# Kernel tuning notes

Hardware: AMD Instinct MI355X
Metric: run time of the kernel (lower is better)

Reference implementation:

```python
import jax, jax.numpy as jnp
import numpy as np

N, E, G, H = 4096, 8192, 64, 128  # nodes, edges, graphs, hidden dim
NODE_DIM, EDGE_DIM = 11, 5


def _linear_params(key, fan_in, fan_out):
    kw, kb = jax.random.split(key)
    s = 1.0 / np.sqrt(fan_in)
    w = jax.random.uniform(kw, (fan_in, fan_out), minval=-s, maxval=s, dtype=jnp.float32)
    b = jax.random.uniform(kb, (fan_out,), minval=-s, maxval=s, dtype=jnp.float32)
    return w, b


def setup_inputs() -> dict:
    key = jax.random.key(0)
    ks = jax.random.split(key, 10)
    x = jax.random.normal(ks[0], (N, NODE_DIM), dtype=jnp.float32)
    edge_attr = jax.random.normal(ks[1], (E, EDGE_DIM), dtype=jnp.float32)
    edge_index = jax.random.randint(ks[2], (2, E), 0, N, dtype=jnp.int64)
    batch = jnp.sort(jax.random.randint(ks[3], (N,), 0, G, dtype=jnp.int64))
    # preprocess MLP: node_dim -> 128 -> 128
    p1_w, p1_b = _linear_params(ks[4], NODE_DIM, H)
    p2_w, p2_b = _linear_params(ks[5], H, H)
    # edge net: edge_dim -> 128 -> 256 -> 128 -> 128*128 (ReLU between, none after last)
    e1_w, e1_b = _linear_params(ks[6], EDGE_DIM, 128)
    e2_w, e2_b = _linear_params(ks[7], 128, 256)
    e3_w, e3_b = _linear_params(ks[8], 256, 128)
    e4_w, e4_b = _linear_params(ks[9], 128, H * H)
    return {"x": x, "edge_attr": edge_attr, "edge_index": edge_index, "batch": batch,
            "p1_w": p1_w, "p1_b": p1_b, "p2_w": p2_w, "p2_b": p2_b,
            "e1_w": e1_w, "e1_b": e1_b, "e2_w": e2_w, "e2_b": e2_b,
            "e3_w": e3_w, "e3_b": e3_b, "e4_w": e4_w, "e4_b": e4_b}


def reference(x, edge_attr, edge_index, batch,
              p1_w, p1_b, p2_w, p2_b,
              e1_w, e1_b, e2_w, e2_b, e3_w, e3_b, e4_w, e4_b):
    # node preprocess MLP (maps 11-dim features to 128 so NNConv dims are consistent)
    h = jax.nn.relu(x @ p1_w + p1_b) @ p2_w + p2_b  # [N, H]
    # edge network -> per-edge weight matrix [E, H, H]
    e = jax.nn.relu(edge_attr @ e1_w + e1_b)
    e = jax.nn.relu(e @ e2_w + e2_b)
    e = jax.nn.relu(e @ e3_w + e3_b)
    W = (e @ e4_w + e4_b).reshape(E, H, H)
    # NNConv (root_weight=False, bias=False, aggr='mean'):
    src, dst = edge_index[0], edge_index[1]
    msg = jnp.einsum('ei,eio->eo', h[src], W)  # gather + per-edge matmul, [E, H]
    agg = jax.ops.segment_sum(msg, dst, num_segments=N)
    cnt = jax.ops.segment_sum(jnp.ones((E,), msg.dtype), dst, num_segments=N)
    h_out = agg / jnp.maximum(cnt, 1.0)[:, None]  # scatter-mean, [N, H]
    # global add pool over graphs
    pooled = jax.ops.segment_sum(h_out, batch, num_segments=G)  # [G, H]
    return pooled
```

## Files before the change

kernel.cpp:

```cpp
#include <hip/hip_runtime.h>
#include <stdint.h>
#include <stddef.h>

typedef unsigned short ushort_t;
typedef __attribute__((ext_vector_type(8))) short short8;
typedef __attribute__((ext_vector_type(4))) short short4v;
typedef __attribute__((ext_vector_type(4))) float f32x4;

#define GL2LDS(gsrc, ldst) \
  __builtin_amdgcn_global_load_lds((const __attribute__((address_space(1))) void*)(gsrc), \
                                   (__attribute__((address_space(3))) void*)(ldst), 16, 0, 0)

__device__ __forceinline__ float bf2f(ushort_t u) {
  union { unsigned int i; float f; } v; v.i = ((unsigned int)u) << 16; return v.f;
}
__device__ __forceinline__ ushort_t f2bf(float f) {
  unsigned int u = __builtin_bit_cast(unsigned int, f);
  unsigned int r = (u + 0x7fffu + ((u >> 16) & 1u)) >> 16;
  return (ushort_t)r;
}

__global__ void k_front(const float* __restrict__ e4w, const float* __restrict__ e4b,
                        ushort_t* __restrict__ e4wT,
                        const float* __restrict__ e2w, ushort_t* __restrict__ w2h,
                        ushort_t* __restrict__ w2l,
                        const float* __restrict__ e3w, ushort_t* __restrict__ w3h,
                        ushort_t* __restrict__ w3l,
                        const float* __restrict__ x, const float* __restrict__ p1w,
                        const float* __restrict__ p1b, const float* __restrict__ p2w,
                        const float* __restrict__ p2b, ushort_t* __restrict__ h_node,
                        const int* __restrict__ eidx, float* __restrict__ cnt) {
  __shared__ char smem[128 * 65 * 4];
  int bid = blockIdx.x, tid = threadIdx.x;

  if (bid < 258) {
    float (*t)[65] = (float(*)[65])smem;
    int c0 = bid * 64;
    for (int it = 0; it < 32; ++it) {
      int idx = it * 256 + tid;
      int cc = idx >> 7, oo = idx & 127;
      int c = c0 + cc;
      float v = (c < 16384) ? e4w[(size_t)c * 128 + oo] : e4b[(size_t)(c - 16384) * 128 + oo];
      t[oo][cc] = v;
    }
    __syncthreads();
    for (int it = 0; it < 32; ++it) {
      int idx = it * 256 + tid;
      int oo = idx >> 6, cc = idx & 63;
      e4wT[(size_t)oo * 16512 + c0 + cc] = f2bf(t[oo][cc]);
    }
  } else if (bid < 274) {
    int id = (bid - 258) * 256 + tid;
    int cf = id >> 8, ks = (id >> 6) & 3, ln = id & 63;
    int n = cf * 16 + (ln & 15);
    int k0 = (ks * 4 + (ln >> 4)) * 8;
    short8 ph, pl;
#pragma unroll
    for (int q = 0; q < 8; ++q) {
      float v = e2w[(size_t)(k0 + q) * 256 + n];
      ushort_t hb = f2bf(v);
      ph[q] = (short)hb;
      pl[q] = (short)f2bf(v - bf2f(hb));
    }
    *(short8*)(w2h + (size_t)id * 8) = ph;
    *(short8*)(w2l + (size_t)id * 8) = pl;
  } else if (bid < 290) {
    int id = (bid - 274) * 256 + tid;
    int cf = id >> 9, ks = (id >> 6) & 7, ln = id & 63;
    int n = cf * 16 + (ln & 15);
    int k0 = (ks * 4 + (ln >> 4)) * 8;
    short8 ph, pl;
#pragma unroll
    for (int q = 0; q < 8; ++q) {
      float v = e3w[(size_t)(k0 + q) * 128 + n];
      ushort_t hb = f2bf(v);
      ph[q] = (short)hb;
      pl[q] = (short)f2bf(v - bf2f(hb));
    }
    *(short8*)(w3h + (size_t)id * 8) = ph;
    *(short8*)(w3l + (size_t)id * 8) = pl;
  } else if (bid < 802) {
    float (*xs)[12] = (float(*)[12])smem;
    float (*t1)[128] = (float(*)[128])(smem + 8 * 12 * 4);
    int n0 = (bid - 290) * 8;
    if (tid < 88) { int n = tid / 11, j = tid % 11; xs[n][j] = x[(size_t)(n0 + n) * 11 + j]; }
    __syncthreads();
    for (int it = 0; it < 4; ++it) {
      int p = it * 256 + tid;
      int n = p >> 7, o = p & 127;
      float a = p1b[o];
#pragma unroll
      for (int j = 0; j < 11; ++j) a += xs[n][j] * p1w[j * 128 + o];
      t1[n][o] = fmaxf(a, 0.f);
    }
    __syncthreads();
    {
      int o = tid & 127, nb = tid >> 7;
      float a0 = p2b[o], a1_ = a0, a2_ = a0, a3_ = a0;
      for (int k4 = 0; k4 < 32; ++k4) {
        float w0 = p2w[(k4 * 4 + 0) * 128 + o];
        float w1 = p2w[(k4 * 4 + 1) * 128 + o];
        float w2 = p2w[(k4 * 4 + 2) * 128 + o];
        float w3 = p2w[(k4 * 4 + 3) * 128 + o];
        float4 v0 = *(const float4*)&t1[nb + 0][k4 * 4];
        float4 v1 = *(const float4*)&t1[nb + 2][k4 * 4];
        float4 v2 = *(const float4*)&t1[nb + 4][k4 * 4];
        float4 v3 = *(const float4*)&t1[nb + 6][k4 * 4];
        a0 += v0.x * w0 + v0.y * w1 + v0.z * w2 + v0.w * w3;
        a1_ += v1.x * w0 + v1.y * w1 + v1.z * w2 + v1.w * w3;
        a2_ += v2.x * w0 + v2.y * w1 + v2.z * w2 + v2.w * w3;
        a3_ += v3.x * w0 + v3.y * w1 + v3.z * w2 + v3.w * w3;
      }
      h_node[(size_t)(n0 + nb + 0) * 128 + o] = f2bf(a0);
      h_node[(size_t)(n0 + nb + 2) * 128 + o] = f2bf(a1_);
      h_node[(size_t)(n0 + nb + 4) * 128 + o] = f2bf(a2_);
      h_node[(size_t)(n0 + nb + 6) * 128 + o] = f2bf(a3_);
    }
  } else {
    int e = (bid - 802) * 256 + tid;
    atomicAdd(&cnt[eidx[8192 + e]], 1.0f);
  }
}

__global__ void k_mlp(const float* __restrict__ ea,
                      const float* __restrict__ e1w, const float* __restrict__ e1b,
                      const ushort_t* __restrict__ w2h, const ushort_t* __restrict__ w2l,
                      const float* __restrict__ e2b,
                      const ushort_t* __restrict__ w3h, const ushort_t* __restrict__ w3l,
                      const float* __restrict__ e3b,
                      float* __restrict__ e3Tf) {
  __shared__ float eas[32][6];
  __shared__ ushort_t a1h[32 * 136], a1l[32 * 136];
  __shared__ ushort_t a2h[32 * 264], a2l[32 * 264];
  __shared__ float a3t[128 * 40];

  int tid = threadIdx.x;
  int w = tid >> 6, ln = tid & 63, g = ln >> 4, l15 = ln & 15;
  int e0 = blockIdx.x * 32;

  if (tid < 160) { int n = tid / 5, j = tid % 5; eas[n][j] = ea[(size_t)(e0 + n) * 5 + j]; }
  __syncthreads();

  {
    int n = tid >> 4, ob = (tid & 15) * 8;
    float acc1[8];
    float4 ba = *(const float4*)(e1b + ob);
    float4 bb = *(const float4*)(e1b + ob + 4);
    acc1[0] = ba.x; acc1[1] = ba.y; acc1[2] = ba.z; acc1[3] = ba.w;
    acc1[4] = bb.x; acc1[5] = bb.y; acc1[6] = bb.z; acc1[7] = bb.w;
#pragma unroll
    for (int j = 0; j < 5; ++j) {
      float aj = eas[n][j];
      float4 wa = *(const float4*)(e1w + j * 128 + ob);
      float4 wb = *(const float4*)(e1w + j * 128 + ob + 4);
      acc1[0] = fmaf(aj, wa.x, acc1[0]); acc1[1] = fmaf(aj, wa.y, acc1[1]);
      acc1[2] = fmaf(aj, wa.z, acc1[2]); acc1[3] = fmaf(aj, wa.w, acc1[3]);
      acc1[4] = fmaf(aj, wb.x, acc1[4]); acc1[5] = fmaf(aj, wb.y, acc1[5]);
      acc1[6] = fmaf(aj, wb.z, acc1[6]); acc1[7] = fmaf(aj, wb.w, acc1[7]);
    }
    short8 ph, pl;
#pragma unroll
    for (int q = 0; q < 8; ++q) {
      float v = fmaxf(acc1[q], 0.f);
      ushort_t hb = f2bf(v);
      ph[q] = (short)hb;
      pl[q] = (short)f2bf(v - bf2f(hb));
    }
    int addr = n * 136 + ob;
    *(short8*)(a1h + addr) = ph;
    *(short8*)(a1l + addr) = pl;
  }
  __syncthreads();

  {
    f32x4 acc2[2][2];
#pragma unroll
    for (int rf = 0; rf < 2; ++rf)
#pragma unroll
      for (int cf = 0; cf < 2; ++cf) acc2[rf][cf] = (f32x4){0.f, 0.f, 0.f, 0.f};
    short8 ah[2][4], al[2][4];
#pragma unroll
    for (int rf = 0; rf < 2; ++rf)
#pragma unroll
      for (int ks = 0; ks < 4; ++ks) {
        int row = rf * 16 + l15;
        int addr = row * 136 + (ks * 4 + g) * 8;
        ah[rf][ks] = *(const short8*)(a1h + addr);
        al[rf][ks] = *(const short8*)(a1l + addr);
      }
#pragma unroll
    for (int ks = 0; ks < 4; ++ks) {
#pragma unroll
      for (int cfi = 0; cfi < 2; ++cfi) {
        int cf = w * 2 + cfi;
        size_t poff = (size_t)(((cf * 4 + ks) << 6) + ln) * 8;
        short8 bh = *(const short8*)(w2h + poff);
        short8 bl = *(const short8*)(w2l + poff);
#pragma unroll
        for (int rf = 0; rf < 2; ++rf) {
          acc2[rf][cfi] = __builtin_amdgcn_mfma_f32_16x16x32_bf16(ah[rf][ks], bh, acc2[rf][cfi], 0, 0, 0);
          acc2[rf][cfi] = __builtin_amdgcn_mfma_f32_16x16x32_bf16(al[rf][ks], bh, acc2[rf][cfi], 0, 0, 0);
          acc2[rf][cfi] = __builtin_amdgcn_mfma_f32_16x16x32_bf16(ah[rf][ks], bl, acc2[rf][cfi], 0, 0, 0);
        }
      }
    }
#pragma unroll
    for (int rf = 0; rf < 2; ++rf)
#pragma unroll
      for (int cfi = 0; cfi < 2; ++cfi) {
        int col = (w * 2 + cfi) * 16 + l15;
        float b = e2b[col];
#pragma unroll
        for (int r2 = 0; r2 < 4; ++r2) {
          int row = rf * 16 + g * 4 + r2;
          float v = fmaxf(acc2[rf][cfi][r2] + b, 0.f);
          ushort_t hb = f2bf(v);
          int addr = row * 264 + col;
          a2h[addr] = hb;
          a2l[addr] = f2bf(v - bf2f(hb));
        }
      }
  }
  __syncthreads();

  {
    f32x4 acc3[2];
    acc3[0] = (f32x4){0.f, 0.f, 0.f, 0.f};
    acc3[1] = (f32x4){0.f, 0.f, 0.f, 0.f};
#pragma unroll
    for (int ks = 0; ks < 8; ++ks) {
      short8 a2hf[2], a2lf[2];
#pragma unroll
      for (int rf = 0; rf < 2; ++rf) {
        int row = rf * 16 + l15;
        int addr = row * 264 + (ks * 4 + g) * 8;
        a2hf[rf] = *(const short8*)(a2h + addr);
        a2lf[rf] = *(const short8*)(a2l + addr);
      }
      size_t poff = (size_t)(((w * 8 + ks) << 6) + ln) * 8;
      short8 bh = *(const short8*)(w3h + poff);
      short8 bl = *(const short8*)(w3l + poff);
#pragma unroll
      for (int rf = 0; rf < 2; ++rf) {
        acc3[rf] = __builtin_amdgcn_mfma_f32_16x16x32_bf16(a2hf[rf], bh, acc3[rf], 0, 0, 0);
        acc3[rf] = __builtin_amdgcn_mfma_f32_16x16x32_bf16(a2lf[rf], bh, acc3[rf], 0, 0, 0);
        acc3[rf] = __builtin_amdgcn_mfma_f32_16x16x32_bf16(a2hf[rf], bl, acc3[rf], 0, 0, 0);
      }
    }
    int col = w * 16 + l15;
    float b = e3b[col];
#pragma unroll
    for (int rf = 0; rf < 2; ++rf)
#pragma unroll
      for (int r2 = 0; r2 < 4; ++r2) {
        int row = rf * 16 + g * 4 + r2;
        float v = fmaxf(acc3[rf][r2] + b, 0.f);
        a3t[col * 40 + row] = v;
      }
  }
  __syncthreads();

  {
    int o = tid >> 2, eq = (tid & 3) * 8;
    float4 q0 = *(const float4*)(a3t + o * 40 + eq);
    float4 q1 = *(const float4*)(a3t + o * 40 + eq + 4);
    *(float4*)(e3Tf + (size_t)o * 8192 + e0 + eq) = q0;
    *(float4*)(e3Tf + (size_t)o * 8192 + e0 + eq + 4) = q1;
  }
}

__launch_bounds__(512, 1)
__global__ void k_gemm(const ushort_t* __restrict__ h_node, const int* __restrict__ eidx,
                       const float* __restrict__ e3Tf,
                       const ushort_t* __restrict__ e4wT, float* __restrict__ agg) {
  __shared__ ushort_t bufA[16384];
  __shared__ float e3s[32 * 128];
  __shared__ int dsts[128];

  int tid = threadIdx.x;
  int w = tid >> 6, ln = tid & 63;
  int g = ln >> 4, l15 = ln & 15;
  int bid = blockIdx.x;
  int mt = bid >> 2, s = bid & 3;
  int e0 = mt * 128;
  int t0 = s * 32;
  int nt = (s == 3) ? 33 : 32;

  if (tid < 128) dsts[tid] = eidx[8192 + e0 + tid];
  {
#pragma unroll
    for (int it = 0; it < 4; ++it) {
      int chunk = it * 512 + tid;
      int r = chunk >> 4;
      int Gt = (chunk & 15) ^ (r & 15);
      int se = eidx[e0 + r];
      GL2LDS(h_node + (size_t)se * 128 + Gt * 8, (char*)&bufA[0] + (it * 512 + w * 64) * 16);
    }
#pragma unroll
    for (int it = 0; it < 2; ++it) {
      int chunk = it * 512 + tid;
      int tl = chunk >> 5, cc = chunk & 31;
      GL2LDS(e3Tf + (size_t)(t0 + tl) * 8192 + e0 + cc * 4,
             (char*)&e3s[0] + (it * 512 + w * 64) * 16);
    }
  }
  asm volatile("s_waitcnt vmcnt(0)" ::: "memory");
  __builtin_amdgcn_s_barrier();
  asm volatile("" ::: "memory");

  short8 afr[8][4];
#pragma unroll
  for (int rf = 0; rf < 8; ++rf)
#pragma unroll
    for (int ks = 0; ks < 4; ++ks) {
      int row = rf * 16 + l15;
      int gr = (ks * 4 + g) ^ (row & 15);
      afr[rf][ks] = *(const short8*)((const char*)&bufA[0] + row * 256 + gr * 16);
    }

  f32x4 acc[8];
#pragma unroll
  for (int rf = 0; rf < 8; ++rf) acc[rf] = (f32x4){0.f, 0.f, 0.f, 0.f};

  const f32x4 zero4 = {0.f, 0.f, 0.f, 0.f};
  int nrow = w * 16 + l15;

  const ushort_t* brow = e4wT + (size_t)nrow * 16512 + (size_t)t0 * 128;
  short8 bcur[4], bnxt[4];
#pragma unroll
  for (int ks = 0; ks < 4; ++ks) bcur[ks] = *(const short8*)(brow + (ks * 4 + g) * 8);
  brow += 128;

  for (int tl = 0; tl < nt; ++tl) {
    int tg = t0 + tl;

    if (tl + 1 < nt) {
#pragma unroll
      for (int ks = 0; ks < 4; ++ks) bnxt[ks] = *(const short8*)(brow + (ks * 4 + g) * 8);
      brow += 128;
    }

    f32x4 part[8];
#pragma unroll
    for (int rf = 0; rf < 8; ++rf)
      part[rf] = __builtin_amdgcn_mfma_f32_16x16x32_bf16(afr[rf][0], bcur[0], zero4, 0, 0, 0);
#pragma unroll
    for (int ks = 1; ks < 4; ++ks)
#pragma unroll
      for (int rf = 0; rf < 8; ++rf)
        part[rf] = __builtin_amdgcn_mfma_f32_16x16x32_bf16(afr[rf][ks], bcur[ks], part[rf], 0, 0, 0);

    if (tg < 128) {
#pragma unroll
      for (int rf = 0; rf < 8; ++rf) {
        float4 ev = *(const float4*)&e3s[tl * 128 + rf * 16 + g * 4];
        acc[rf][0] = fmaf(ev.x, part[rf][0], acc[rf][0]);
        acc[rf][1] = fmaf(ev.y, part[rf][1], acc[rf][1]);
        acc[rf][2] = fmaf(ev.z, part[rf][2], acc[rf][2]);
        acc[rf][3] = fmaf(ev.w, part[rf][3], acc[rf][3]);
      }
    } else {
#pragma unroll
      for (int rf = 0; rf < 8; ++rf)
#pragma unroll
        for (int r2 = 0; r2 < 4; ++r2) acc[rf][r2] += part[rf][r2];
    }

    if (tl + 1 < nt) {
#pragma unroll
      for (int ks = 0; ks < 4; ++ks) bcur[ks] = bnxt[ks];
    }
  }

#pragma unroll
  for (int rf = 0; rf < 8; ++rf)
#pragma unroll
    for (int r2 = 0; r2 < 4; ++r2) {
      int row = rf * 16 + g * 4 + r2;
      int d = dsts[row];
      atomicAdd(&agg[(size_t)d * 128 + nrow], acc[rf][r2]);
    }
}

__device__ __forceinline__ int lbound(const int* a, int n, int v) {
  int lo = 0, hi = n;
  while (lo < hi) { int m = (lo + hi) >> 1; if (a[m] < v) lo = m + 1; else hi = m; }
  return lo;
}

__global__ void k_pool(const float* __restrict__ agg, const float* __restrict__ cnt,
                       const int* __restrict__ batch, float* __restrict__ out) {
  int gph = blockIdx.x, o = threadIdx.x;
  int lo = lbound(batch, 4096, gph);
  int hi = lbound(batch, 4096, gph + 1);
  float a = 0.f;
  for (int n = lo; n < hi; ++n) a += agg[(size_t)n * 128 + o] / fmaxf(cnt[n], 1.0f);
  out[(size_t)gph * 128 + o] = a;
}

extern "C" void kernel_launch(void* const* d_in, const int* in_sizes, int n_in,
                              void* d_out, int out_size, void* d_ws, size_t ws_size,
                              hipStream_t stream) {
  (void)in_sizes; (void)n_in; (void)out_size; (void)ws_size;
  const float* x   = (const float*)d_in[0];
  const float* ea  = (const float*)d_in[1];
  const int*   ei  = (const int*)d_in[2];
  const int*   bat = (const int*)d_in[3];
  const float* p1w = (const float*)d_in[4];  const float* p1b = (const float*)d_in[5];
  const float* p2w = (const float*)d_in[6];  const float* p2b = (const float*)d_in[7];
  const float* e1w = (const float*)d_in[8];  const float* e1b = (const float*)d_in[9];
  const float* e2w = (const float*)d_in[10]; const float* e2b = (const float*)d_in[11];
  const float* e3w = (const float*)d_in[12]; const float* e3b = (const float*)d_in[13];
  const float* e4w = (const float*)d_in[14]; const float* e4b = (const float*)d_in[15];

  char* ws = (char*)d_ws;
  ushort_t* e4wT   = (ushort_t*)(ws + 0);
  ushort_t* h_node = (ushort_t*)(ws + 4227072);
  float*    e3Tf   = (float*)(ws + 5275648);
  float*    agg    = (float*)(ws + 9469952);
  float*    cnt    = (float*)(ws + 11567104);
  ushort_t* w2h    = (ushort_t*)(ws + 11583488);
  ushort_t* w2l    = (ushort_t*)(ws + 11649024);
  ushort_t* w3h    = (ushort_t*)(ws + 11714560);
  ushort_t* w3l    = (ushort_t*)(ws + 11780096);

  hipMemsetAsync(ws + 9469952, 0, 2097152 + 16384, stream);

  k_front <<<834,  256, 0, stream>>>(e4w, e4b, e4wT, e2w, w2h, w2l, e3w, w3h, w3l,
                                     x, p1w, p1b, p2w, p2b, h_node, ei, cnt);
  k_mlp   <<<256,  512, 0, stream>>>(ea, e1w, e1b, w2h, w2l, e2b,
                                     w3h, w3l, e3b, e3Tf);
  k_gemm  <<<256,  512, 0, stream>>>(h_node, ei, e3Tf, e4wT, agg);
  k_pool  <<<64,   128, 0, stream>>>(agg, cnt, bat, (float*)d_out);
}
```

Baseline: 180.0 us.

## Pre-pack e4 weights into MFMA fragment order and deepen B prefetch

The front kernel now converts the e4 weight matrix to bf16 and writes it directly in per-lane MFMA fragment order, one tile per block, instead of as a strided transpose. The gemm kernel can then load each lane's B fragments as contiguous, fully coalesced 16-byte chunks rather than strided row reads. B prefetch also goes from double to triple buffering, so global loads are issued two tiles ahead. The cost is more registers in a kernel already holding large A fragments, and a front-kernel transpose done through shared memory with 2-byte accesses.

```diff
diff --git a/kernel.cpp b/kernel.cpp
--- a/kernel.cpp
+++ b/kernel.cpp
@@ -21,7 +21,7 @@
 }
 
 __global__ void k_front(const float* __restrict__ e4w, const float* __restrict__ e4b,
-                        ushort_t* __restrict__ e4wT,
+                        ushort_t* __restrict__ e4wP,
                         const float* __restrict__ e2w, ushort_t* __restrict__ w2h,
                         ushort_t* __restrict__ w2l,
                         const float* __restrict__ e3w, ushort_t* __restrict__ w3h,
@@ -30,27 +30,39 @@
                         const float* __restrict__ p1b, const float* __restrict__ p2w,
                         const float* __restrict__ p2b, ushort_t* __restrict__ h_node,
                         const int* __restrict__ eidx, float* __restrict__ cnt) {
-  __shared__ char smem[128 * 65 * 4];
+  __shared__ char smem[128 * 130 * 2];
   int bid = blockIdx.x, tid = threadIdx.x;
 
-  if (bid < 258) {
-    float (*t)[65] = (float(*)[65])smem;
-    int c0 = bid * 64;
-    for (int it = 0; it < 32; ++it) {
+  if (bid < 129) {
+    int tg = bid;
+    const float* src = (tg < 128) ? (e4w + (size_t)tg * 16384) : e4b;
+    ushort_t (*t)[130] = (ushort_t(*)[130])smem;
+#pragma unroll
+    for (int it = 0; it < 16; ++it) {
       int idx = it * 256 + tid;
-      int cc = idx >> 7, oo = idx & 127;
-      int c = c0 + cc;
-      float v = (c < 16384) ? e4w[(size_t)c * 128 + oo] : e4b[(size_t)(c - 16384) * 128 + oo];
-      t[oo][cc] = v;
+      int cl = idx >> 5, o4 = (idx & 31) * 4;
+      float4 v = *(const float4*)(src + cl * 128 + o4);
+      t[cl][o4 + 0] = f2bf(v.x);
+      t[cl][o4 + 1] = f2bf(v.y);
+      t[cl][o4 + 2] = f2bf(v.z);
+      t[cl][o4 + 3] = f2bf(v.w);
     }
     __syncthreads();
-    for (int it = 0; it < 32; ++it) {
-      int idx = it * 256 + tid;
-      int oo = idx >> 6, cc = idx & 63;
-      e4wT[(size_t)oo * 16512 + c0 + cc] = f2bf(t[oo][cc]);
-    }
-  } else if (bid < 274) {
-    int id = (bid - 258) * 256 + tid;
+    ushort_t* dst = e4wP + (size_t)tg * 16384;
+#pragma unroll
+    for (int it = 0; it < 8; ++it) {
+      int fs = it * 256 + tid;
+      int fid = fs >> 6, ln = fs & 63;
+      int cf = fid >> 2, ks = fid & 3;
+      int o = cf * 16 + (ln & 15);
+      int k0 = (ks * 4 + (ln >> 4)) * 8;
+      short8 p;
+#pragma unroll
+      for (int q = 0; q < 8; ++q) p[q] = (short)t[k0 + q][o];
+      *(short8*)(dst + (size_t)fs * 8) = p;
+    }
+  } else if (bid < 145) {
+    int id = (bid - 129) * 256 + tid;
     int cf = id >> 8, ks = (id >> 6) & 3, ln = id & 63;
     int n = cf * 16 + (ln & 15);
     int k0 = (ks * 4 + (ln >> 4)) * 8;
@@ -64,8 +76,8 @@
     }
     *(short8*)(w2h + (size_t)id * 8) = ph;
     *(short8*)(w2l + (size_t)id * 8) = pl;
-  } else if (bid < 290) {
-    int id = (bid - 274) * 256 + tid;
+  } else if (bid < 161) {
+    int id = (bid - 145) * 256 + tid;
     int cf = id >> 9, ks = (id >> 6) & 7, ln = id & 63;
     int n = cf * 16 + (ln & 15);
     int k0 = (ks * 4 + (ln >> 4)) * 8;
@@ -79,10 +91,10 @@
     }
     *(short8*)(w3h + (size_t)id * 8) = ph;
     *(short8*)(w3l + (size_t)id * 8) = pl;
-  } else if (bid < 802) {
+  } else if (bid < 673) {
     float (*xs)[12] = (float(*)[12])smem;
     float (*t1)[128] = (float(*)[128])(smem + 8 * 12 * 4);
-    int n0 = (bid - 290) * 8;
+    int n0 = (bid - 161) * 8;
     if (tid < 88) { int n = tid / 11, j = tid % 11; xs[n][j] = x[(size_t)(n0 + n) * 11 + j]; }
     __syncthreads();
     for (int it = 0; it < 4; ++it) {
@@ -117,7 +129,7 @@
       h_node[(size_t)(n0 + nb + 6) * 128 + o] = f2bf(a3_);
     }
   } else {
-    int e = (bid - 802) * 256 + tid;
+    int e = (bid - 673) * 256 + tid;
     atomicAdd(&cnt[eidx[8192 + e]], 1.0f);
   }
 }
@@ -272,7 +284,7 @@
 __launch_bounds__(512, 1)
 __global__ void k_gemm(const ushort_t* __restrict__ h_node, const int* __restrict__ eidx,
                        const float* __restrict__ e3Tf,
-                       const ushort_t* __restrict__ e4wT, float* __restrict__ agg) {
+                       const ushort_t* __restrict__ e4wP, float* __restrict__ agg) {
   __shared__ ushort_t bufA[16384];
   __shared__ float e3s[32 * 128];
   __shared__ int dsts[128];
@@ -325,30 +337,34 @@
   const f32x4 zero4 = {0.f, 0.f, 0.f, 0.f};
   int nrow = w * 16 + l15;
 
-  const ushort_t* brow = e4wT + (size_t)nrow * 16512 + (size_t)t0 * 128;
-  short8 bcur[4], bnxt[4];
-#pragma unroll
-  for (int ks = 0; ks < 4; ++ks) bcur[ks] = *(const short8*)(brow + (ks * 4 + g) * 8);
-  brow += 128;
+  const size_t TSTR = 32 * 64 * 8;
+  const ushort_t* bp = e4wP + (((size_t)t0 * 32 + w * 4) * 64 + ln) * 8;
+  short8 b0[4], b1[4], b2[4];
+#pragma unroll
+  for (int ks = 0; ks < 4; ++ks) b0[ks] = *(const short8*)(bp + ks * 512);
+  bp += TSTR;
+#pragma unroll
+  for (int ks = 0; ks < 4; ++ks) b1[ks] = *(const short8*)(bp + ks * 512);
+  bp += TSTR;
 
   for (int tl = 0; tl < nt; ++tl) {
     int tg = t0 + tl;
 
-    if (tl + 1 < nt) {
-#pragma unroll
-      for (int ks = 0; ks < 4; ++ks) bnxt[ks] = *(const short8*)(brow + (ks * 4 + g) * 8);
-      brow += 128;
+    if (tl + 2 < nt) {
+#pragma unroll
+      for (int ks = 0; ks < 4; ++ks) b2[ks] = *(const short8*)(bp + ks * 512);
+      bp += TSTR;
     }
 
     f32x4 part[8];
 #pragma unroll
     for (int rf = 0; rf < 8; ++rf)
-      part[rf] = __builtin_amdgcn_mfma_f32_16x16x32_bf16(afr[rf][0], bcur[0], zero4, 0, 0, 0);
+      part[rf] = __builtin_amdgcn_mfma_f32_16x16x32_bf16(afr[rf][0], b0[0], zero4, 0, 0, 0);
 #pragma unroll
     for (int ks = 1; ks < 4; ++ks)
 #pragma unroll
       for (int rf = 0; rf < 8; ++rf)
-        part[rf] = __builtin_amdgcn_mfma_f32_16x16x32_bf16(afr[rf][ks], bcur[ks], part[rf], 0, 0, 0);
+        part[rf] = __builtin_amdgcn_mfma_f32_16x16x32_bf16(afr[rf][ks], b0[ks], part[rf], 0, 0, 0);
 
     if (tg < 128) {
 #pragma unroll
@@ -366,10 +382,8 @@
         for (int r2 = 0; r2 < 4; ++r2) acc[rf][r2] += part[rf][r2];
     }
 
-    if (tl + 1 < nt) {
-#pragma unroll
-      for (int ks = 0; ks < 4; ++ks) bcur[ks] = bnxt[ks];
-    }
+#pragma unroll
+    for (int ks = 0; ks < 4; ++ks) { b0[ks] = b1[ks]; b1[ks] = b2[ks]; }
   }
 
 #pragma unroll
@@ -414,7 +428,7 @@
   const float* e4w = (const float*)d_in[14]; const float* e4b = (const float*)d_in[15];
 
   char* ws = (char*)d_ws;
-  ushort_t* e4wT   = (ushort_t*)(ws + 0);
+  ushort_t* e4wP   = (ushort_t*)(ws + 0);
   ushort_t* h_node = (ushort_t*)(ws + 4227072);
   float*    e3Tf   = (float*)(ws + 5275648);
   float*    agg    = (float*)(ws + 9469952);
@@ -426,10 +440,10 @@
 
   hipMemsetAsync(ws + 9469952, 0, 2097152 + 16384, stream);
 
-  k_front <<<834,  256, 0, stream>>>(e4w, e4b, e4wT, e2w, w2h, w2l, e3w, w3h, w3l,
+  k_front <<<705,  256, 0, stream>>>(e4w, e4b, e4wP, e2w, w2h, w2l, e3w, w3h, w3l,
                                      x, p1w, p1b, p2w, p2b, h_node, ei, cnt);
   k_mlp   <<<256,  512, 0, stream>>>(ea, e1w, e1b, w2h, w2l, e2b,
                                      w3h, w3l, e3b, e3Tf);
-  k_gemm  <<<256,  512, 0, stream>>>(h_node, ei, e3Tf, e4wT, agg);
+  k_gemm  <<<256,  512, 0, stream>>>(h_node, ei, e3Tf, e4wP, agg);
   k_pool  <<<64,   128, 0, stream>>>(agg, cnt, bat, (float*)d_out);
 }
```

After: 205.2 us. 14.0% more time.
